# Kernel optimization log

Measured on AMD Instinct MI355X. Metric: run time of the kernel, lower is better.

The kernel has to match this reference:

```python
import math
import jax, jax.numpy as jnp
import numpy as np

SPECIAL = 4; LABEL_ID = 3
ACT_V = 64; TIME_V = 32
VOCAB = SPECIAL + ACT_V + TIME_V  # 100
D = 1024; L = 4; H = 16; DH = D // H
B = 4; T = 1024
CAT0, CAT1 = 16, 32
N_NUM = 4; N_TIME = 6


def _posenc(t, d):
    pos = np.arange(t)[:, None]
    i = np.arange(d // 2)[None, :]
    ang = pos / np.power(10000.0, 2.0 * i / d)
    pe = np.zeros((t, d), dtype=np.float32)
    pe[:, 0::2] = np.sin(ang)
    pe[:, 1::2] = np.cos(ang)
    return jnp.asarray(pe)


def _ln(x, g, b):
    m = jnp.mean(x, -1, keepdims=True)
    v = jnp.mean((x - m) ** 2, -1, keepdims=True)
    return (x - m) * jax.lax.rsqrt(v + 1e-5) * g + b


def setup_inputs() -> dict:
    key = jax.random.key(0)
    ks = iter(jax.random.split(key, 64))
    nrm = lambda shape, s=0.02: jax.random.normal(next(ks), shape, jnp.float32) * s
    inp = {}
    inp['tokens'] = jax.random.randint(next(ks), (B, T), 0, VOCAB)
    inp['cat_feats'] = jax.random.randint(next(ks), (B, T, 2), 0, CAT0)
    inp['num_feats'] = jax.random.normal(next(ks), (B, T, N_NUM), jnp.float32)
    inp['time_feats'] = jax.random.normal(next(ks), (B, T, N_TIME), jnp.float32)
    inp['attention_mask'] = jnp.ones((B, T), jnp.int32)
    inp['loss_mask'] = jax.random.randint(next(ks), (B, T), 0, 2).astype(bool)
    inp['task_ids'] = jax.random.randint(next(ks), (B,), 0, 2)
    # embedder params
    inp['E'] = nrm((VOCAB, D))
    inp['cat_emb0'] = nrm((CAT0, D))
    inp['cat_emb1'] = nrm((CAT1, D))
    inp['Wn'] = nrm((N_NUM, D)); inp['bn'] = jnp.zeros((D,), jnp.float32)
    inp['Wt'] = nrm((N_TIME, D)); inp['bt'] = jnp.zeros((D,), jnp.float32)
    # backbone params, stacked over layers
    inp['Wqkv'] = nrm((L, D, 3 * D)); inp['bqkv'] = jnp.zeros((L, 3 * D), jnp.float32)
    inp['Wo'] = nrm((L, D, D)); inp['bo'] = jnp.zeros((L, D), jnp.float32)
    inp['ln1_g'] = jnp.ones((L, D), jnp.float32); inp['ln1_b'] = jnp.zeros((L, D), jnp.float32)
    inp['W1'] = nrm((L, D, 4 * D)); inp['b1'] = jnp.zeros((L, 4 * D), jnp.float32)
    inp['W2'] = nrm((L, 4 * D, D)); inp['b2'] = jnp.zeros((L, D), jnp.float32)
    inp['ln2_g'] = jnp.ones((L, D), jnp.float32); inp['ln2_b'] = jnp.zeros((L, D), jnp.float32)
    inp['lnf_g'] = jnp.ones((D,), jnp.float32); inp['lnf_b'] = jnp.zeros((D,), jnp.float32)
    # heads
    inp['W_next'] = nrm((D, ACT_V)); inp['b_next'] = jnp.zeros((ACT_V,), jnp.float32)
    inp['W_timeh'] = nrm((D, TIME_V)); inp['b_timeh'] = jnp.zeros((TIME_V,), jnp.float32)
    inp['task_embed'] = nrm((2, D))
    inp['tied_scale_act'] = jnp.asarray(0.5, jnp.float32)
    inp['tied_scale_time'] = jnp.asarray(0.5, jnp.float32)
    inp['copy_scale_act'] = jnp.asarray(0.5, jnp.float32)
    inp['copy_scale_time'] = jnp.asarray(0.5, jnp.float32)
    return inp


def reference(tokens, cat_feats, num_feats, time_feats, attention_mask, loss_mask, task_ids,
              E, cat_emb0, cat_emb1, Wn, bn, Wt, bt,
              Wqkv, bqkv, Wo, bo, ln1_g, ln1_b, W1, b1, W2, b2, ln2_g, ln2_b, lnf_g, lnf_b,
              W_next, b_next, W_timeh, b_timeh, task_embed,
              tied_scale_act, tied_scale_time, copy_scale_act, copy_scale_time):
    Bq, Tq = tokens.shape
    # ---- EventEmbedder: sum of token/categorical/numeric/time embeddings + PE
    x = E[tokens] + cat_emb0[cat_feats[..., 0]] + cat_emb1[cat_feats[..., 1]]
    x = x + num_feats @ Wn + bn + time_feats @ Wt + bt
    x = x + _posenc(Tq, D)
    # ---- task conditioning
    x = x + task_embed[task_ids][:, None, :]
    # ---- causal + key-padding mask
    pad = attention_mask == 0
    causal = jnp.triu(jnp.ones((Tq, Tq), bool), 1)
    neg = jnp.where(causal[None, None] | pad[:, None, None, :], -1e9, 0.0).astype(x.dtype)
    # ---- pre-LN decoder-only transformer
    for l in range(L):
        hln = _ln(x, ln1_g[l], ln1_b[l])
        qkv = hln @ Wqkv[l] + bqkv[l]
        q, k, v = jnp.split(qkv, 3, axis=-1)
        q = q.reshape(Bq, Tq, H, DH); k = k.reshape(Bq, Tq, H, DH); v = v.reshape(Bq, Tq, H, DH)
        sc = jnp.einsum('bqhd,bkhd->bhqk', q, k) / math.sqrt(DH) + neg
        p = jax.nn.softmax(sc, axis=-1)
        a = jnp.einsum('bhqk,bkhd->bqhd', p, v).reshape(Bq, Tq, D)
        x = x + a @ Wo[l] + bo[l]
        hln = _ln(x, ln2_g[l], ln2_b[l])
        x = x + jax.nn.relu(hln @ W1[l] + b1[l]) @ W2[l] + b2[l]
    h = _ln(x, lnf_g, lnf_b)  # [B,T,D]
    # ---- parametric heads
    param_next = h @ W_next + b_next
    param_time = h @ W_timeh + b_timeh
    # ---- weight-tied heads
    W_act = E[SPECIAL:SPECIAL + ACT_V]
    W_tb = E[SPECIAL + ACT_V:SPECIAL + ACT_V + TIME_V]
    tied_act = h @ W_act.T
    tied_time = h @ W_tb.T
    # ---- retrieval/copy head (vectorized gather-matmul-scatter)
    is_label = tokens == LABEL_ID
    value_mask = jnp.pad(is_label[:, :-1], ((0, 0), (1, 0)))  # prev token is <LABEL>
    act_start = SPECIAL; time_start = SPECIAL + ACT_V
    val_act = value_mask & (tokens >= act_start) & (tokens < time_start)
    val_time = value_mask & (tokens >= time_start) & (tokens < time_start + TIME_V)
    sims = jnp.einsum('bqd,bkd->bqk', h, h) / math.sqrt(D)  # all-pairs similarity
    oh_act = jax.nn.one_hot(tokens - act_start, ACT_V, dtype=h.dtype) * val_act[..., None]
    oh_time = jax.nn.one_hot(tokens - time_start, TIME_V, dtype=h.dtype) * val_time[..., None]
    qm = loss_mask[..., None].astype(h.dtype)  # copy logits only at query <LABEL> positions
    copy_act = jnp.einsum('bqk,bkc->bqc', sims, oh_act) * qm
    copy_time = jnp.einsum('bqk,bkc->bqc', sims, oh_time) * qm
    sp = jax.nn.softplus
    activity_logits = param_next + sp(tied_scale_act) * tied_act + sp(copy_scale_act) * copy_act
    time_logits = param_time + sp(tied_scale_time) * tied_time + sp(copy_scale_time) * copy_time
    return activity_logits, time_logits
```

## Files before the change

### kernel.cpp

```cpp
#include <hip/hip_runtime.h>
#include <cstdint>
#include <cstddef>

typedef unsigned short u16;
typedef __attribute__((ext_vector_type(8))) short bf16x8;
typedef __attribute__((ext_vector_type(4))) float f32x4;

#define DMODEL 1024
#define TLEN   1024
#define BATCH  4
#define NHEAD  16

__device__ __forceinline__ float bf2f(u16 u) {
  union { unsigned int i; float f; } x; x.i = ((unsigned int)u) << 16; return x.f;
}
__device__ __forceinline__ u16 f2bf(float f) {
  union { float f; unsigned int i; } x; x.f = f;
  unsigned int r = x.i + 0x7fffu + ((x.i >> 16) & 1u);
  return (u16)(r >> 16);
}
__device__ __forceinline__ void ld8bf(const u16* p, float* f) {
  uint4 u = *(const uint4*)p;
  f[0] = bf2f((u16)(u.x & 0xffff)); f[1] = bf2f((u16)(u.x >> 16));
  f[2] = bf2f((u16)(u.y & 0xffff)); f[3] = bf2f((u16)(u.y >> 16));
  f[4] = bf2f((u16)(u.z & 0xffff)); f[5] = bf2f((u16)(u.z >> 16));
  f[6] = bf2f((u16)(u.w & 0xffff)); f[7] = bf2f((u16)(u.w >> 16));
}
__device__ __forceinline__ void ld4bf(const u16* p, float* f) {
  uint2 u = *(const uint2*)p;
  f[0] = bf2f((u16)(u.x & 0xffff)); f[1] = bf2f((u16)(u.x >> 16));
  f[2] = bf2f((u16)(u.y & 0xffff)); f[3] = bf2f((u16)(u.y >> 16));
}
__device__ __forceinline__ float softplus_f(float x) {
  return (x > 20.f) ? x : log1pf(__expf(x));
}
__device__ __forceinline__ void async_ld16(const void* g, void* l) {
  __builtin_amdgcn_global_load_lds(
      (const __attribute__((address_space(1))) unsigned int*)g,
      (__attribute__((address_space(3))) unsigned int*)l, 16, 0, 0);
}

__global__ void embed_kernel(const int* __restrict__ tokens, const int* __restrict__ cat,
    const float* __restrict__ numf, const float* __restrict__ timef, const int* __restrict__ task_ids,
    const float* __restrict__ E, const float* __restrict__ ce0, const float* __restrict__ ce1,
    const float* __restrict__ Wn, const float* __restrict__ bn, const float* __restrict__ Wtm,
    const float* __restrict__ btm, const float* __restrict__ taskemb, float* __restrict__ X)
{
  const int bt = blockIdx.x;
  const int b = bt >> 10, t = bt & 1023;
  const int tok = tokens[bt];
  const int c0 = cat[bt * 2 + 0], c1 = cat[bt * 2 + 1];
  const int tk = task_ids[b];
  float nf[4], tf[6];
#pragma unroll
  for (int i = 0; i < 4; ++i) nf[i] = numf[bt * 4 + i];
#pragma unroll
  for (int i = 0; i < 6; ++i) tf[i] = timef[bt * 6 + i];
  const int d0 = threadIdx.x * 4;
  float v[4];
  {
    float4 a = *(const float4*)(E + (size_t)tok * DMODEL + d0);
    float4 b2 = *(const float4*)(ce0 + (size_t)c0 * DMODEL + d0);
    float4 c2 = *(const float4*)(ce1 + (size_t)c1 * DMODEL + d0);
    float4 d2 = *(const float4*)(taskemb + (size_t)tk * DMODEL + d0);
    float4 e2 = *(const float4*)(bn + d0);
    float4 f2 = *(const float4*)(btm + d0);
    v[0] = a.x + b2.x + c2.x + d2.x + e2.x + f2.x;
    v[1] = a.y + b2.y + c2.y + d2.y + e2.y + f2.y;
    v[2] = a.z + b2.z + c2.z + d2.z + e2.z + f2.z;
    v[3] = a.w + b2.w + c2.w + d2.w + e2.w + f2.w;
  }
#pragma unroll
  for (int i = 0; i < 4; ++i) {
    float4 w = *(const float4*)(Wn + (size_t)i * DMODEL + d0);
    v[0] += nf[i] * w.x; v[1] += nf[i] * w.y; v[2] += nf[i] * w.z; v[3] += nf[i] * w.w;
  }
#pragma unroll
  for (int i = 0; i < 6; ++i) {
    float4 w = *(const float4*)(Wtm + (size_t)i * DMODEL + d0);
    v[0] += tf[i] * w.x; v[1] += tf[i] * w.y; v[2] += tf[i] * w.z; v[3] += tf[i] * w.w;
  }
#pragma unroll
  for (int j = 0; j < 4; ++j) {
    const int d = d0 + j;
    const int i2 = d >> 1;
    const float ang = (float)t * expf(-0.017988946f * (float)i2);
    v[j] += (d & 1) ? cosf(ang) : sinf(ang);
  }
  *(float4*)(X + (size_t)bt * DMODEL + d0) = make_float4(v[0], v[1], v[2], v[3]);
}

__global__ void ln_kernel(const float* __restrict__ X, const float* __restrict__ g,
                          const float* __restrict__ be, u16* __restrict__ O)
{
  const int row = blockIdx.x * 4 + (threadIdx.x >> 6);
  const int lane = threadIdx.x & 63;
  const float* xr = X + (size_t)row * DMODEL;
  float v[16];
  float s = 0.f, s2 = 0.f;
#pragma unroll
  for (int i = 0; i < 4; ++i) {
    float4 t4 = *(const float4*)(xr + lane * 4 + i * 256);
    v[i*4+0] = t4.x; v[i*4+1] = t4.y; v[i*4+2] = t4.z; v[i*4+3] = t4.w;
    s  += t4.x + t4.y + t4.z + t4.w;
    s2 += t4.x*t4.x + t4.y*t4.y + t4.z*t4.z + t4.w*t4.w;
  }
#pragma unroll
  for (int off = 32; off > 0; off >>= 1) {
    s  += __shfl_xor(s, off, 64);
    s2 += __shfl_xor(s2, off, 64);
  }
  const float mean = s * (1.f / 1024.f);
  const float var  = s2 * (1.f / 1024.f) - mean * mean;
  const float rs   = rsqrtf(var + 1e-5f);
  u16* orow = O + (size_t)row * DMODEL;
#pragma unroll
  for (int i = 0; i < 4; ++i) {
    float4 gg = *(const float4*)(g + lane * 4 + i * 256);
    float4 bb = *(const float4*)(be + lane * 4 + i * 256);
    float r0 = (v[i*4+0] - mean) * rs * gg.x + bb.x;
    float r1 = (v[i*4+1] - mean) * rs * gg.y + bb.y;
    float r2 = (v[i*4+2] - mean) * rs * gg.z + bb.z;
    float r3 = (v[i*4+3] - mean) * rs * gg.w + bb.w;
    uint2 o2;
    o2.x = (unsigned)f2bf(r0) | ((unsigned)f2bf(r1) << 16);
    o2.y = (unsigned)f2bf(r2) | ((unsigned)f2bf(r3) << 16);
    *(uint2*)(orow + lane * 4 + i * 256) = o2;
  }
}

__global__ void transpose_f2b(const float* __restrict__ in, u16* __restrict__ out,
                              int R, int C, int ldin)
{
  __shared__ u16 tile[64][65];
  const int c0 = blockIdx.x * 64, r0 = blockIdx.y * 64;
  const int tx = threadIdx.x & 15, ty = threadIdx.x >> 4;
#pragma unroll
  for (int i = 0; i < 4; ++i) {
    const int r = ty + i * 16;
    float4 f = *(const float4*)(in + (size_t)(r0 + r) * ldin + c0 + tx * 4);
    tile[r][tx*4+0] = f2bf(f.x);
    tile[r][tx*4+1] = f2bf(f.y);
    tile[r][tx*4+2] = f2bf(f.z);
    tile[r][tx*4+3] = f2bf(f.w);
  }
  __syncthreads();
#pragma unroll
  for (int i = 0; i < 4; ++i) {
    const int rr = ty + i * 16;
    uint2 o;
    o.x = (unsigned)tile[tx*4+0][rr] | ((unsigned)tile[tx*4+1][rr] << 16);
    o.y = (unsigned)tile[tx*4+2][rr] | ((unsigned)tile[tx*4+3][rr] << 16);
    *(uint2*)(out + (size_t)(c0 + rr) * R + r0 + tx * 4) = o;
  }
}

template<bool RESID, bool RELU, bool OUTBF, bool QKVMODE>
__global__ void gemm_bt(const u16* __restrict__ A, const u16* __restrict__ Bt,
                        const float* __restrict__ bias, const float* __restrict__ resid,
                        void* __restrict__ outp, u16* __restrict__ vt,
                        int M, int N, int K, int lda)
{
  __shared__ u16 As[128 * 32];
  __shared__ u16 Bs[128 * 32];
  const int tid = threadIdx.x;
  const int wave = tid >> 6, lane = tid & 63;
  const int m0 = blockIdx.y * 128, n0 = blockIdx.x * 128;
  const int wm = (wave >> 1) * 64, wn = (wave & 1) * 64;
  const int lrow = lane & 15, quad = lane >> 4;
  f32x4 acc[4][4] = {};
  for (int kt = 0; kt < K; kt += 32) {
    __syncthreads();
#pragma unroll
    for (int p = 0; p < 2; ++p) {
      const int idx = p * 256 + tid;
      const int r = idx >> 2, cc = (idx & 3) << 3;
      const int lofs = (p * 256 + wave * 64) << 3;
      async_ld16(A + (size_t)(m0 + r) * lda + kt + cc, As + lofs);
      async_ld16(Bt + (size_t)(n0 + r) * K + kt + cc, Bs + lofs);
    }
    __syncthreads();
    bf16x8 af[4], bfr[4];
#pragma unroll
    for (int i = 0; i < 4; ++i) {
      af[i]  = *(const bf16x8*)(As + (wm + i * 16 + lrow) * 32 + quad * 8);
      bfr[i] = *(const bf16x8*)(Bs + (wn + i * 16 + lrow) * 32 + quad * 8);
    }
#pragma unroll
    for (int i = 0; i < 4; ++i)
#pragma unroll
      for (int j = 0; j < 4; ++j)
        acc[i][j] = __builtin_amdgcn_mfma_f32_16x16x32_bf16(af[i], bfr[j], acc[i][j], 0, 0, 0);
  }
#pragma unroll
  for (int i = 0; i < 4; ++i) {
#pragma unroll
    for (int j = 0; j < 4; ++j) {
      const int col = n0 + wn + j * 16 + lrow;
      const float bv = bias ? bias[col] : 0.f;
#pragma unroll
      for (int r = 0; r < 4; ++r) {
        const int row = m0 + wm + i * 16 + quad * 4 + r;
        float vv = acc[i][j][r] + bv;
        if (RESID) vv += resid[(size_t)row * N + col];
        if (RELU)  vv = fmaxf(vv, 0.f);
        if (QKVMODE) {
          if (col < 2048) {
            ((u16*)outp)[(size_t)row * 2048 + col] = f2bf(vv);
          } else {
            const int hd = col - 2048;
            const int b = row >> 10, t = row & 1023;
            vt[(((size_t)b * 16 + (hd >> 6)) * 64 + (hd & 63)) * 1024 + t] = f2bf(vv);
          }
        } else if (OUTBF) {
          ((u16*)outp)[(size_t)row * N + col] = f2bf(vv);
        } else {
          ((float*)outp)[(size_t)row * N + col] = vv;
        }
      }
    }
  }
}

__launch_bounds__(256, 4)
__global__ void attn_flash(u16* __restrict__ QK, const u16* __restrict__ VT,
                           const int* __restrict__ amask)
{
  __shared__ u16 Pw[4][16 * 72];
  const int tid  = threadIdx.x;
  const int wave = tid >> 6, lane = tid & 63;
  const int l15  = lane & 15, quad = lane >> 4;
  const int qb = blockIdx.x, h = blockIdx.y, b = blockIdx.z;
  const int qbase = qb * 64 + wave * 16;

  u16* bq = QK + (size_t)b * TLEN * 2048 + h * 64;
  const u16* Kb = bq + 1024;
  const u16* Vb = VT + ((size_t)b * 16 + h) * 64 * 1024;
  const int* am = amask + b * TLEN;

  bf16x8 aq0 = *(const bf16x8*)(bq + (size_t)(qbase + l15) * 2048 + quad * 8);
  bf16x8 aq1 = *(const bf16x8*)(bq + (size_t)(qbase + l15) * 2048 + 32 + quad * 8);

  f32x4 o[4] = {};
  float m[4], l[4];
#pragma unroll
  for (int r = 0; r < 4; ++r) { m[r] = -1e30f; l[r] = 0.f; }

  u16* myP = Pw[wave];

  for (int kb = 0; kb <= qb; ++kb) {
    const int kt = kb * 64;
    float p[4][4];
#pragma unroll
    for (int j = 0; j < 4; ++j) {
      const u16* kr = Kb + (size_t)(kt + j * 16 + l15) * 2048;
      bf16x8 bk0 = *(const bf16x8*)(kr + quad * 8);
      bf16x8 bk1 = *(const bf16x8*)(kr + 32 + quad * 8);
      f32x4 sacc = {};
      sacc = __builtin_amdgcn_mfma_f32_16x16x32_bf16(aq0, bk0, sacc, 0, 0, 0);
      sacc = __builtin_amdgcn_mfma_f32_16x16x32_bf16(aq1, bk1, sacc, 0, 0, 0);
      const float negm = (am[kt + j * 16 + l15] == 0) ? -1e9f : 0.f;
#pragma unroll
      for (int r = 0; r < 4; ++r) p[j][r] = sacc[r] * 0.125f + negm;
    }
    if (kb == qb) {
#pragma unroll
      for (int j = 0; j < 4; ++j) {
        const int colL = j * 16 + l15;
#pragma unroll
        for (int r = 0; r < 4; ++r) {
          const int rowL = wave * 16 + quad * 4 + r;
          if (colL > rowL) p[j][r] = -1e30f;
        }
      }
    }
#pragma unroll
    for (int r = 0; r < 4; ++r) {
      float mm = fmaxf(fmaxf(p[0][r], p[1][r]), fmaxf(p[2][r], p[3][r]));
      mm = fmaxf(mm, __shfl_xor(mm, 1));
      mm = fmaxf(mm, __shfl_xor(mm, 2));
      mm = fmaxf(mm, __shfl_xor(mm, 4));
      mm = fmaxf(mm, __shfl_xor(mm, 8));
      const float nm = fmaxf(m[r], mm);
      const float al = __expf(m[r] - nm);
      m[r] = nm;
      float ls = 0.f;
#pragma unroll
      for (int j = 0; j < 4; ++j) { p[j][r] = __expf(p[j][r] - nm); ls += p[j][r]; }
      ls += __shfl_xor(ls, 1); ls += __shfl_xor(ls, 2);
      ls += __shfl_xor(ls, 4); ls += __shfl_xor(ls, 8);
      l[r] = l[r] * al + ls;
#pragma unroll
      for (int n = 0; n < 4; ++n) o[n][r] *= al;
    }
#pragma unroll
    for (int j = 0; j < 4; ++j)
#pragma unroll
      for (int r = 0; r < 4; ++r)
        myP[(quad * 4 + r) * 72 + j * 16 + l15] = f2bf(p[j][r]);
    __asm__ volatile("s_waitcnt lgkmcnt(0)" ::: "memory");
    bf16x8 pa0 = *(const bf16x8*)(myP + l15 * 72 + quad * 8);
    bf16x8 pa1 = *(const bf16x8*)(myP + l15 * 72 + 32 + quad * 8);
#pragma unroll
    for (int n = 0; n < 4; ++n) {
      const u16* vrow = Vb + (size_t)(n * 16 + l15) * 1024 + kt;
      bf16x8 bv0 = *(const bf16x8*)(vrow + quad * 8);
      bf16x8 bv1 = *(const bf16x8*)(vrow + 32 + quad * 8);
      o[n] = __builtin_amdgcn_mfma_f32_16x16x32_bf16(pa0, bv0, o[n], 0, 0, 0);
      o[n] = __builtin_amdgcn_mfma_f32_16x16x32_bf16(pa1, bv1, o[n], 0, 0, 0);
    }
  }
#pragma unroll
  for (int r = 0; r < 4; ++r) {
    const float inv = (l[r] > 0.f) ? 1.f / l[r] : 0.f;
    u16* po = bq + (size_t)(qbase + quad * 4 + r) * 2048;
#pragma unroll
    for (int n = 0; n < 4; ++n)
      po[n * 16 + l15] = f2bf(o[n][r] * inv);
  }
}

__global__ void foldM(const float* __restrict__ E, const float* __restrict__ Wnext,
                      const float* __restrict__ Wtimeh, const float* __restrict__ bnext,
                      const float* __restrict__ btimeh, const float* __restrict__ s_act,
                      const float* __restrict__ s_time, u16* __restrict__ MT, float* __restrict__ biasC)
{
  const int c = blockIdx.x;
  const float sa = softplus_f(s_act[0]);
  const float st = softplus_f(s_time[0]);
  const int d0 = threadIdx.x * 4;
#pragma unroll
  for (int j = 0; j < 4; ++j) {
    const int d = d0 + j;
    float v = 0.f;
    if (c < 64)      v = Wnext[(size_t)d * 64 + c] + sa * E[(size_t)(4 + c) * DMODEL + d];
    else if (c < 96) v = Wtimeh[(size_t)d * 32 + (c - 64)] + st * E[(size_t)(68 + c - 64) * DMODEL + d];
    MT[(size_t)c * DMODEL + d] = f2bf(v);
  }
  if (threadIdx.x == 0) {
    float bv = 0.f;
    if (c < 64) bv = bnext[c];
    else if (c < 96) bv = btimeh[c - 64];
    biasC[c] = bv;
  }
}

__global__ void gbuild(const int* __restrict__ tokens, const u16* __restrict__ HB,
                       float* __restrict__ G, int* __restrict__ Gnz)
{
  const int b = blockIdx.x;
  __shared__ int cls[1024];
  for (int i = threadIdx.x; i < 96 * 1024; i += 256) G[(size_t)b * 96 * 1024 + i] = 0.f;
  for (int k = threadIdx.x; k < 1024; k += 256) {
    int c = -1;
    if (k > 0 && tokens[b * 1024 + k - 1] == 3) {
      const int tok = tokens[b * 1024 + k];
      if (tok >= 4 && tok < 68) c = tok - 4;
      else if (tok >= 68 && tok < 100) c = 64 + (tok - 68);
    }
    cls[k] = c;
  }
  if (threadIdx.x < 96) Gnz[b * 96 + threadIdx.x] = 0;
  __syncthreads();
  const int d0 = threadIdx.x * 4;
  for (int k = 1; k < 1024; ++k) {
    const int c = cls[k];
    if (c < 0) continue;
    if (threadIdx.x == 0) Gnz[b * 96 + c] = 1;
    float* gr = G + ((size_t)b * 96 + c) * 1024 + d0;
    float hv[4];
    ld4bf(HB + ((size_t)b * 1024 + k) * 1024 + d0, hv);
#pragma unroll
    for (int j = 0; j < 4; ++j) gr[j] += hv[j];
  }
}

__global__ void final_kernel(const u16* __restrict__ HB, const float* __restrict__ OUT96,
                             const float* __restrict__ G, const int* __restrict__ Gnz,
                             const int* __restrict__ lossm, const float* __restrict__ s_ca,
                             const float* __restrict__ s_ct, float* __restrict__ out_act,
                             float* __restrict__ out_time)
{
  __shared__ float hs[1024];
  const int row = blockIdx.x;
  const int b = row >> 10;
  const u16* hrow = HB + (size_t)row * 1024;
  {
    const int i = threadIdx.x;
    float hv[8];
    ld8bf(hrow + i * 8, hv);
#pragma unroll
    for (int j = 0; j < 8; ++j) hs[i * 8 + j] = hv[j];
  }
  __syncthreads();
  const int c = threadIdx.x;
  if (c >= 96) return;
  float val = OUT96[(size_t)row * 128 + c];
  if (lossm[row] != 0 && Gnz[b * 96 + c] != 0) {
    const float4* gr = (const float4*)(G + ((size_t)b * 96 + c) * 1024);
    float dot = 0.f;
    for (int d4 = 0; d4 < 256; ++d4) {
      float4 gg = gr[d4];
      dot += hs[d4*4+0]*gg.x + hs[d4*4+1]*gg.y + hs[d4*4+2]*gg.z + hs[d4*4+3]*gg.w;
    }
    const float sc = (c < 64) ? softplus_f(s_ca[0]) : softplus_f(s_ct[0]);
    val += sc * dot * (1.f / 32.f);
  }
  if (c < 64) out_act[(size_t)row * 64 + c] = val;
  else        out_time[(size_t)row * 32 + (c - 64)] = val;
}

extern "C" void kernel_launch(void* const* d_in, const int* in_sizes, int n_in,
                              void* d_out, int out_size, void* d_ws, size_t ws_size,
                              hipStream_t stream)
{
  const int*   tokens = (const int*)d_in[0];
  const int*   cat    = (const int*)d_in[1];
  const float* numf   = (const float*)d_in[2];
  const float* timef  = (const float*)d_in[3];
  const int*   amask  = (const int*)d_in[4];
  const int*   lossm  = (const int*)d_in[5];
  const int*   task   = (const int*)d_in[6];
  const float* E      = (const float*)d_in[7];
  const float* ce0    = (const float*)d_in[8];
  const float* ce1    = (const float*)d_in[9];
  const float* Wn     = (const float*)d_in[10];
  const float* bn     = (const float*)d_in[11];
  const float* Wtm    = (const float*)d_in[12];
  const float* btm    = (const float*)d_in[13];
  const float* Wqkv   = (const float*)d_in[14];
  const float* bqkv   = (const float*)d_in[15];
  const float* Wo     = (const float*)d_in[16];
  const float* bo     = (const float*)d_in[17];
  const float* ln1g   = (const float*)d_in[18];
  const float* ln1b   = (const float*)d_in[19];
  const float* W1     = (const float*)d_in[20];
  const float* b1     = (const float*)d_in[21];
  const float* W2     = (const float*)d_in[22];
  const float* b2     = (const float*)d_in[23];
  const float* ln2g   = (const float*)d_in[24];
  const float* ln2b   = (const float*)d_in[25];
  const float* lnfg   = (const float*)d_in[26];
  const float* lnfb   = (const float*)d_in[27];
  const float* Wnext  = (const float*)d_in[28];
  const float* bnext  = (const float*)d_in[29];
  const float* Wtimeh = (const float*)d_in[30];
  const float* btimeh = (const float*)d_in[31];
  const float* taskemb= (const float*)d_in[32];
  const float* ts_act = (const float*)d_in[33];
  const float* ts_time= (const float*)d_in[34];
  const float* cs_act = (const float*)d_in[35];
  const float* cs_time= (const float*)d_in[36];

  float* out_act  = (float*)d_out;
  float* out_time = out_act + (size_t)BATCH * TLEN * 64;

  uint8_t* ws = (uint8_t*)d_ws;
  float* X   = (float*)(ws);
  u16*   XB  = (u16*)(ws + (16ull << 20));
  u16*   SCR = (u16*)(ws + (24ull << 20));
  u16*   VT  = (u16*)(ws + (40ull << 20));
  u16*   WT  = (u16*)(ws + (48ull << 20));
  u16*   MT    = (u16*)  (ws + (24ull << 20));
  float* BIASC = (float*)(ws + (24ull << 20) + (512ull << 10));
  float* OUT96 = (float*)(ws + (25ull << 20));
  float* G     = (float*)(ws + (28ull << 20));
  int*   GNZ   = (int*)  (ws + (30ull << 20));

  embed_kernel<<<4096, 256, 0, stream>>>(tokens, cat, numf, timef, task, E, ce0, ce1,
                                         Wn, bn, Wtm, btm, taskemb, X);

  for (int l = 0; l < 4; ++l) {
    ln_kernel<<<1024, 256, 0, stream>>>(X, ln1g + l * 1024, ln1b + l * 1024, XB);
    transpose_f2b<<<dim3(48, 16), 256, 0, stream>>>(Wqkv + (size_t)l * 1024 * 3072, WT, 1024, 3072, 3072);
    gemm_bt<false, false, true, true><<<dim3(24, 32), 256, 0, stream>>>(XB, WT, bqkv + l * 3072, nullptr, SCR, VT, 4096, 3072, 1024, 1024);
    attn_flash<<<dim3(16, 16, 4), 256, 0, stream>>>(SCR, VT, amask);
    transpose_f2b<<<dim3(16, 16), 256, 0, stream>>>(Wo + (size_t)l * 1024 * 1024, WT, 1024, 1024, 1024);
    gemm_bt<true, false, false, false><<<dim3(8, 32), 256, 0, stream>>>(SCR , WT, bo + l * 1024, X, X, nullptr, 4096, 1024, 1024, 2048);
    ln_kernel<<<1024, 256, 0, stream>>>(X, ln2g + l * 1024, ln2b + l * 1024, XB);
    for (int nh = 0; nh < 2; ++nh) {
      transpose_f2b<<<dim3(32, 16), 256, 0, stream>>>(W1 + (size_t)l * 1024 * 4096 + nh * 2048, WT, 1024, 2048, 4096);
      gemm_bt<false, true, true, false><<<dim3(16, 32), 256, 0, stream>>>(XB, WT, b1 + l * 4096 + nh * 2048, nullptr, SCR, nullptr, 4096, 2048, 1024, 1024);
      transpose_f2b<<<dim3(16, 32), 256, 0, stream>>>(W2 + ((size_t)l * 4096 + nh * 2048) * 1024, WT, 2048, 1024, 1024);
      gemm_bt<true, false, false, false><<<dim3(8, 32), 256, 0, stream>>>(SCR, WT, nh == 0 ? (b2 + l * 1024) : nullptr, X, X, nullptr, 4096, 1024, 2048, 2048);
    }
  }

  ln_kernel<<<1024, 256, 0, stream>>>(X, lnfg, lnfb, XB);
  foldM<<<128, 256, 0, stream>>>(E, Wnext, Wtimeh, bnext, btimeh, ts_act, ts_time, MT, BIASC);
  gemm_bt<false, false, false, false><<<dim3(1, 32), 256, 0, stream>>>(XB, MT, BIASC, nullptr, OUT96, nullptr, 4096, 128, 1024, 1024);
  gbuild<<<4, 256, 0, stream>>>(tokens, XB, G, GNZ);
  final_kernel<<<4096, 128, 0, stream>>>(XB, OUT96, G, GNZ, lossm, cs_act, cs_time, out_act, out_time);
}
```

Before: 1.873 ms.

## Transpose attention MFMA layout and widen key tiles to 128 with per-wave causal skipping

Rewrites the flash attention inner loop to compute S^T (keys × queries), so each lane owns one query row. This drops the 16-lane shuffle reductions for max and sum in favor of two cross-quad shuffles. Key blocks grow from 64 to 128, and the causal bound is now per wave (qlast), so fully masked 16-key tiles and 32-key PV chunks are skipped. P is written to LDS with packed 64-bit stores, and the output uses packed stores. The cost is more registers for the 8x4 score tile and branchier loop bodies.

Result: no change. 1.898 ms (+1.3%).

```diff
diff --git a/kernel.cpp b/kernel.cpp
--- a/kernel.cpp
+++ b/kernel.cpp
@@ -226,97 +226,104 @@
 __global__ void attn_flash(u16* __restrict__ QK, const u16* __restrict__ VT,
                            const int* __restrict__ amask)
 {
-  __shared__ u16 Pw[4][16 * 72];
-  const int tid  = threadIdx.x;
+  __shared__ u16 Pw[4][16 * 136];
+  const int tid = threadIdx.x;
   const int wave = tid >> 6, lane = tid & 63;
-  const int l15  = lane & 15, quad = lane >> 4;
+  const int l15 = lane & 15, quad = lane >> 4;
   const int qb = blockIdx.x, h = blockIdx.y, b = blockIdx.z;
   const int qbase = qb * 64 + wave * 16;
+  const int qlast = qbase + 15;
 
   u16* bq = QK + (size_t)b * TLEN * 2048 + h * 64;
   const u16* Kb = bq + 1024;
   const u16* Vb = VT + ((size_t)b * 16 + h) * 64 * 1024;
   const int* am = amask + b * TLEN;
 
-  bf16x8 aq0 = *(const bf16x8*)(bq + (size_t)(qbase + l15) * 2048 + quad * 8);
-  bf16x8 aq1 = *(const bf16x8*)(bq + (size_t)(qbase + l15) * 2048 + 32 + quad * 8);
+  const size_t qrow = (size_t)(qbase + l15) * 2048;
+  const int myq = qbase + l15;
+  bf16x8 fq0 = *(const bf16x8*)(bq + qrow + quad * 8);
+  bf16x8 fq1 = *(const bf16x8*)(bq + qrow + 32 + quad * 8);
 
   f32x4 o[4] = {};
-  float m[4], l[4];
-#pragma unroll
-  for (int r = 0; r < 4; ++r) { m[r] = -1e30f; l[r] = 0.f; }
-
+  float m = -1e30f, l = 0.f;
   u16* myP = Pw[wave];
-
-  for (int kb = 0; kb <= qb; ++kb) {
-    const int kt = kb * 64;
-    float p[4][4];
-#pragma unroll
-    for (int j = 0; j < 4; ++j) {
-      const u16* kr = Kb + (size_t)(kt + j * 16 + l15) * 2048;
-      bf16x8 bk0 = *(const bf16x8*)(kr + quad * 8);
-      bf16x8 bk1 = *(const bf16x8*)(kr + 32 + quad * 8);
-      f32x4 sacc = {};
-      sacc = __builtin_amdgcn_mfma_f32_16x16x32_bf16(aq0, bk0, sacc, 0, 0, 0);
-      sacc = __builtin_amdgcn_mfma_f32_16x16x32_bf16(aq1, bk1, sacc, 0, 0, 0);
-      const float negm = (am[kt + j * 16 + l15] == 0) ? -1e9f : 0.f;
-#pragma unroll
-      for (int r = 0; r < 4; ++r) p[j][r] = sacc[r] * 0.125f + negm;
-    }
-    if (kb == qb) {
-#pragma unroll
-      for (int j = 0; j < 4; ++j) {
-        const int colL = j * 16 + l15;
-#pragma unroll
-        for (int r = 0; r < 4; ++r) {
-          const int rowL = wave * 16 + quad * 4 + r;
-          if (colL > rowL) p[j][r] = -1e30f;
-        }
+  const int nkb = qlast / 128 + 1;
+
+  for (int kb = 0; kb < nkb; ++kb) {
+    const int kt = kb * 128;
+    float s[8][4];
+#pragma unroll
+    for (int jt = 0; jt < 8; ++jt) {
+      const int keyb = kt + jt * 16;
+      if (keyb > qlast) continue;
+      const u16* kr = Kb + (size_t)(keyb + l15) * 2048;
+      bf16x8 k0 = *(const bf16x8*)(kr + quad * 8);
+      bf16x8 k1 = *(const bf16x8*)(kr + 32 + quad * 8);
+      f32x4 sa = {};
+      sa = __builtin_amdgcn_mfma_f32_16x16x32_bf16(k0, fq0, sa, 0, 0, 0);
+      sa = __builtin_amdgcn_mfma_f32_16x16x32_bf16(k1, fq1, sa, 0, 0, 0);
+      const int4 amv = *(const int4*)(am + keyb + quad * 4);
+      const int k0i = keyb + quad * 4;
+#pragma unroll
+      for (int r = 0; r < 4; ++r) {
+        const int amr = (r == 0) ? amv.x : (r == 1) ? amv.y : (r == 2) ? amv.z : amv.w;
+        float v = sa[r] * 0.125f + ((amr == 0) ? -1e9f : 0.f);
+        if (k0i + r > myq) v = -1e30f;
+        s[jt][r] = v;
       }
     }
-#pragma unroll
-    for (int r = 0; r < 4; ++r) {
-      float mm = fmaxf(fmaxf(p[0][r], p[1][r]), fmaxf(p[2][r], p[3][r]));
-      mm = fmaxf(mm, __shfl_xor(mm, 1));
-      mm = fmaxf(mm, __shfl_xor(mm, 2));
-      mm = fmaxf(mm, __shfl_xor(mm, 4));
-      mm = fmaxf(mm, __shfl_xor(mm, 8));
-      const float nm = fmaxf(m[r], mm);
-      const float al = __expf(m[r] - nm);
-      m[r] = nm;
-      float ls = 0.f;
-#pragma unroll
-      for (int j = 0; j < 4; ++j) { p[j][r] = __expf(p[j][r] - nm); ls += p[j][r]; }
-      ls += __shfl_xor(ls, 1); ls += __shfl_xor(ls, 2);
-      ls += __shfl_xor(ls, 4); ls += __shfl_xor(ls, 8);
-      l[r] = l[r] * al + ls;
-#pragma unroll
-      for (int n = 0; n < 4; ++n) o[n][r] *= al;
-    }
-#pragma unroll
-    for (int j = 0; j < 4; ++j)
-#pragma unroll
-      for (int r = 0; r < 4; ++r)
-        myP[(quad * 4 + r) * 72 + j * 16 + l15] = f2bf(p[j][r]);
+    float mm = -1e30f;
+#pragma unroll
+    for (int jt = 0; jt < 8; ++jt) {
+      if (kt + jt * 16 > qlast) continue;
+      mm = fmaxf(mm, fmaxf(fmaxf(s[jt][0], s[jt][1]), fmaxf(s[jt][2], s[jt][3])));
+    }
+    mm = fmaxf(mm, __shfl_xor(mm, 16));
+    mm = fmaxf(mm, __shfl_xor(mm, 32));
+    const float nm = fmaxf(m, mm);
+    const float al = __expf(m - nm);
+    m = nm;
+    float ls = 0.f;
+#pragma unroll
+    for (int jt = 0; jt < 8; ++jt) {
+      uint2 w2;
+      if (kt + jt * 16 <= qlast) {
+        float p0 = __expf(s[jt][0] - nm), p1 = __expf(s[jt][1] - nm);
+        float p2 = __expf(s[jt][2] - nm), p3 = __expf(s[jt][3] - nm);
+        ls += (p0 + p1) + (p2 + p3);
+        w2.x = (unsigned)f2bf(p0) | ((unsigned)f2bf(p1) << 16);
+        w2.y = (unsigned)f2bf(p2) | ((unsigned)f2bf(p3) << 16);
+      } else {
+        w2.x = 0; w2.y = 0;
+      }
+      *(uint2*)(myP + l15 * 136 + jt * 16 + quad * 4) = w2;
+    }
+#pragma unroll
+    for (int n = 0; n < 4; ++n) {
+      o[n][0] *= al; o[n][1] *= al; o[n][2] *= al; o[n][3] *= al;
+    }
+    ls += __shfl_xor(ls, 16);
+    ls += __shfl_xor(ls, 32);
+    l = l * al + ls;
     __asm__ volatile("s_waitcnt lgkmcnt(0)" ::: "memory");
-    bf16x8 pa0 = *(const bf16x8*)(myP + l15 * 72 + quad * 8);
-    bf16x8 pa1 = *(const bf16x8*)(myP + l15 * 72 + 32 + quad * 8);
-#pragma unroll
-    for (int n = 0; n < 4; ++n) {
-      const u16* vrow = Vb + (size_t)(n * 16 + l15) * 1024 + kt;
-      bf16x8 bv0 = *(const bf16x8*)(vrow + quad * 8);
-      bf16x8 bv1 = *(const bf16x8*)(vrow + 32 + quad * 8);
-      o[n] = __builtin_amdgcn_mfma_f32_16x16x32_bf16(pa0, bv0, o[n], 0, 0, 0);
-      o[n] = __builtin_amdgcn_mfma_f32_16x16x32_bf16(pa1, bv1, o[n], 0, 0, 0);
-    }
-  }
-#pragma unroll
-  for (int r = 0; r < 4; ++r) {
-    const float inv = (l[r] > 0.f) ? 1.f / l[r] : 0.f;
-    u16* po = bq + (size_t)(qbase + quad * 4 + r) * 2048;
-#pragma unroll
-    for (int n = 0; n < 4; ++n)
-      po[n * 16 + l15] = f2bf(o[n][r] * inv);
+#pragma unroll
+    for (int c = 0; c < 4; ++c) {
+      if (kt + c * 32 > qlast) break;
+      bf16x8 pb = *(const bf16x8*)(myP + l15 * 136 + c * 32 + quad * 8);
+#pragma unroll
+      for (int n = 0; n < 4; ++n) {
+        bf16x8 va = *(const bf16x8*)(Vb + (size_t)(n * 16 + l15) * 1024 + kt + c * 32 + quad * 8);
+        o[n] = __builtin_amdgcn_mfma_f32_16x16x32_bf16(va, pb, o[n], 0, 0, 0);
+      }
+    }
+  }
+  const float inv = (l > 0.f) ? 1.f / l : 0.f;
+#pragma unroll
+  for (int n = 0; n < 4; ++n) {
+    uint2 w2;
+    w2.x = (unsigned)f2bf(o[n][0] * inv) | ((unsigned)f2bf(o[n][1] * inv) << 16);
+    w2.y = (unsigned)f2bf(o[n][2] * inv) | ((unsigned)f2bf(o[n][3] * inv) << 16);
+    *(uint2*)(bq + qrow + n * 16 + quad * 4) = w2;
   }
 }
 
```
